# Performance work log

Hardware: AMD Instinct MI355X
Metric: run time of the kernel (lower is better)

## Reference

```python
import jax, jax.numpy as jnp
import numpy as np
from jax import lax

B, L, M, H = 8, 16, 256, 53
HID, NH, HD = 64, 4, 16  # hidden_size, n_heads, head_dim
ACT = 15  # 3 sub-actions x 5 categories


def _lstm_last(x, Wih, Whh, bih, bhh):
    # x: [N, T, D] batch_first; torch LSTM gate order i,f,g,o. Returns last hidden [N, HID].
    N = x.shape[0]
    h0 = jnp.zeros((N, HID), x.dtype)
    c0 = jnp.zeros((N, HID), x.dtype)
    def step(carry, xt):
        h, c = carry
        g = xt @ Wih.T + bih + h @ Whh.T + bhh
        i, f, gg, o = jnp.split(g, 4, axis=-1)
        c = jax.nn.sigmoid(f) * c + jax.nn.sigmoid(i) * jnp.tanh(gg)
        h = jax.nn.sigmoid(o) * jnp.tanh(c)
        return (h, c), None
    (h, _), _ = lax.scan(step, (h0, c0), x.transpose(1, 0, 2))
    return h


def setup_inputs():
    key = jax.random.key(0)
    ks = jax.random.split(key, 32)
    rn = lambda k, sh: (jax.random.normal(k, sh, jnp.float32) * 0.05)
    Gmat = jax.random.randint(ks[3], (M, M), 0, 2)
    Gmat = Gmat.at[jnp.arange(M), jnp.arange(M)].set(1)  # self-contact so no all-masked row
    return {
        'x_actor': jax.random.normal(ks[0], (B, L, M, H), jnp.float32),
        'x_critic': jax.random.normal(ks[1], (B, L, M, H), jnp.float32),
        'action': jax.random.randint(ks[2], (B, M, 3), 0, 5),
        'Gmat': Gmat,
        'Wa': rn(ks[4], (HID, H)), 'ba': jnp.zeros((HID,), jnp.float32),
        'Wg': rn(ks[5], (HID, H)), 'bg': jnp.zeros((HID,), jnp.float32),
        'Qw': rn(ks[6], (HID, HID)), 'Kw': rn(ks[7], (HID, HID)),
        'W2': rn(ks[8], (HID, 2 * HID)), 'b2': jnp.zeros((HID,), jnp.float32),
        'Wih_a': rn(ks[9], (4 * HID, HID)), 'Whh_a': rn(ks[10], (4 * HID, HID)),
        'bih_a': jnp.zeros((4 * HID,), jnp.float32), 'bhh_a': jnp.zeros((4 * HID,), jnp.float32),
        'Wih_c': rn(ks[11], (4 * HID, HID)), 'Whh_c': rn(ks[12], (4 * HID, HID)),
        'bih_c': jnp.zeros((4 * HID,), jnp.float32), 'bhh_c': jnp.zeros((4 * HID,), jnp.float32),
        'Wma1': rn(ks[13], (HID, HID)), 'bma1': jnp.zeros((HID,), jnp.float32),
        'Wma2': rn(ks[14], (ACT, HID)), 'bma2': jnp.zeros((ACT,), jnp.float32),
        'Wmc1': rn(ks[15], (HID, HID)), 'bmc1': jnp.zeros((HID,), jnp.float32),
        'Wmc2': rn(ks[16], (1, HID)), 'bmc2': jnp.zeros((1,), jnp.float32),
    }


def reference(x_actor, x_critic, action, Gmat, Wa, ba, Wg, bg, Qw, Kw, W2, b2,
              Wih_a, Whh_a, bih_a, bhh_a, Wih_c, Whh_c, bih_c, bhh_c,
              Wma1, bma1, Wma2, bma2, Wmc1, bmc1, Wmc2, bmc2):
    Bb, Ll, Mm, Hh = x_actor.shape
    xa = x_actor.transpose(1, 0, 2, 3).reshape(Ll * Bb, Mm, Hh)
    xc = xa  # original code overwrites x_critic with x_actor (preserved)
    a_lin = xa @ Wa.T + ba                               # [LB, M, HID]
    # --- GAT (GCN2) ---
    s = xc @ Wg.T + bg                                   # [LB, M, HID]
    q = (s @ Qw).reshape(-1, Mm, NH, HD)
    k = (s @ Kw).reshape(-1, Mm, NH, HD)
    s4 = s.reshape(-1, Mm, NH, HD)
    att = jnp.einsum('blhe,bshe->bhls', q, k) / jnp.asarray(128.0, s.dtype) ** 0.5
    att = jnp.where(Gmat > 0, att, jnp.asarray(-9e15, att.dtype))
    att = jax.nn.softmax(att, axis=-1)
    s_out = jnp.einsum('bshe,bhls->blhe', s4, att).reshape(-1, Mm, NH * HD)
    c_feat = jnp.concatenate([s, s_out], axis=-1) @ W2.T + b2  # [LB, M, HID]
    # --- to sequences [B*M, L, HID] ---
    xa_seq = a_lin.reshape(Ll, Bb * Mm, HID).transpose(1, 0, 2)
    xc_seq = c_feat.reshape(Ll, Bb * Mm, HID).transpose(1, 0, 2)
    ah = _lstm_last(xa_seq, Wih_a, Whh_a, bih_a, bhh_a)          # [B*M, HID]
    ch = _lstm_last(xc_seq, Wih_c, Whh_c, bih_c, bhh_c).reshape(Bb, Mm, HID)
    logits = (jnp.tanh(ah @ Wma1.T + bma1) @ Wma2.T + bma2).reshape(Bb, Mm, 3, 5)
    logp = jax.nn.log_softmax(logits, axis=-1)
    lp = jnp.take_along_axis(logp, action[..., None], axis=-1).squeeze(-1)  # [B,M,3]
    ent = -jnp.sum(jnp.exp(logp) * logp, axis=-1)                           # [B,M,3]
    value = jnp.tanh(ch @ Wmc1.T + bmc1) @ Wmc2.T + bmc2                    # [B,M,1]
    return (action, lp.sum(-1), ent.sum(-1), value)
```

## Files before the change

### kernel.cpp

```cpp
#include <hip/hip_runtime.h>
#include <math.h>

#define B_ 8
#define L_ 16
#define M_ 256
#define H_ 53
#define HID_ 64
#define LB_ 128
#define SCALE_ 0.08838834764831845f

typedef __attribute__((ext_vector_type(8))) short bf16x8;
typedef __attribute__((ext_vector_type(4))) float f32x4;

__device__ inline unsigned short f2bf(float f) {
  unsigned u = __builtin_bit_cast(unsigned, f);
  unsigned r = (u + 0x7FFFu + ((u >> 16) & 1u)) >> 16;
  return (unsigned short)r;
}
__device__ inline float sigm(float x) { return __builtin_amdgcn_rcpf(1.f + __expf(-x)); }
__device__ inline float ftanh(float x) { return 1.f - 2.f * __builtin_amdgcn_rcpf(1.f + __expf(2.f * x)); }

__global__ __launch_bounds__(256) void kP_pre(
    const float* __restrict__ Wg, const float* __restrict__ bg,
    const float* __restrict__ Qw, const float* __restrict__ Kw,
    const float* __restrict__ Wih_c, const float* __restrict__ W2,
    const float* __restrict__ b2, const int* __restrict__ Gmat,
    unsigned short* __restrict__ WQ_b, unsigned short* __restrict__ WK_b,
    float* __restrict__ bqk, unsigned short* __restrict__ Wfold_b,
    float* __restrict__ bias_fold, unsigned* __restrict__ gmask) {
  int blk = blockIdx.x, tid = threadIdx.x;
  if (blk < 128) {
    int idx = blk * 256 + tid;
    int n = idx >> 7, t = idx & 127;
    float acc = 0.f;
    for (int e = 0; e < 64; ++e) acc = fmaf(Wih_c[n * 64 + e], W2[e * 128 + t], acc);
    Wfold_b[idx] = f2bf(acc);
  } else if (blk < 160) {
    int idx = (blk - 128) * 256 + tid;
    int which = idx >> 12, n = (idx >> 6) & 63, j = idx & 63;
    const float* Mm = which ? Kw : Qw;
    float acc = 0.f;
    if (j < 53) {
      for (int e = 0; e < 64; ++e) acc = fmaf(Mm[e * 64 + n], Wg[e * 53 + j], acc);
      if (which == 0) acc *= SCALE_;
    }
    (which ? WK_b : WQ_b)[n * 64 + j] = f2bf(acc);
  } else if (blk == 160) {
    if (tid < 128) {
      int which = tid >> 6, n = tid & 63;
      const float* Mm = which ? Kw : Qw;
      float acc = 0.f;
      for (int e = 0; e < 64; ++e) acc = fmaf(bg[e], Mm[e * 64 + n], acc);
      if (which == 0) acc *= SCALE_;
      bqk[tid] = acc;
    }
  } else if (blk == 161) {
    float acc = 0.f;
    for (int e = 0; e < 64; ++e) acc = fmaf(Wih_c[tid * 64 + e], b2[e], acc);
    bias_fold[tid] = acc;
  } else {
    int w = tid >> 6, ln = tid & 63;
    int l = (blk - 162) * 4 + w;
    #pragma unroll
    for (int c = 0; c < 4; ++c) {
      int gv = Gmat[l * 256 + c * 64 + ln];
      unsigned long long msk = __ballot(gv > 0);
      if (ln == 0) {
        gmask[l * 8 + c * 2] = (unsigned)msk;
        gmask[l * 8 + c * 2 + 1] = (unsigned)(msk >> 32);
      }
    }
  }
}

#define XS 68
#define WS 68
#define OS 264
__global__ __launch_bounds__(256, 2) void kA_lin(const float* __restrict__ x,
    const float* __restrict__ Wa, const float* __restrict__ ba,
    const float* __restrict__ Wg, const float* __restrict__ bg,
    const unsigned short* __restrict__ WQ_b, const unsigned short* __restrict__ WK_b,
    const float* __restrict__ bqk,
    unsigned short* __restrict__ a_lin_bf, unsigned short* __restrict__ s_b,
    unsigned short* __restrict__ q_b, unsigned short* __restrict__ k_b,
    unsigned short* __restrict__ sT_b) {
  __shared__ __attribute__((aligned(16))) unsigned short x_lds[64 * XS];
  __shared__ __attribute__((aligned(16))) unsigned short w_lds[256 * WS];
  __shared__ float bias_lds[256];
  __shared__ __attribute__((aligned(16))) unsigned short out_lds[64 * OS];
  int tid = threadIdx.x;
  int row0 = blockIdx.x * 64;
  for (int i = tid; i < 64 * 64; i += 256) {
    int r = i >> 6, j = i & 63;
    int row = row0 + r;
    int lb = row >> 8, m = row & 255;
    int l = lb >> 3, b = lb & 7;
    float v = (j < 53) ? x[((b * L_ + l) * M_ + m) * H_ + j] : 0.f;
    x_lds[r * XS + j] = f2bf(v);
  }
  for (int i = tid; i < 64 * 64; i += 256) {
    int n = i >> 6, j = i & 63;
    w_lds[n * WS + j] = (j < 53) ? f2bf(Wa[n * 53 + j]) : 0;
    w_lds[(64 + n) * WS + j] = (j < 53) ? f2bf(Wg[n * 53 + j]) : 0;
    w_lds[(128 + n) * WS + j] = WQ_b[i];
    w_lds[(192 + n) * WS + j] = WK_b[i];
  }
  {
    float bv;
    if (tid < 64) bv = ba[tid];
    else if (tid < 128) bv = bg[tid - 64];
    else bv = bqk[tid - 128];
    bias_lds[tid] = bv;
  }
  __syncthreads();
  int lane = tid & 63, w = tid >> 6;
  int c16 = lane & 15, q4 = lane >> 4;
  bf16x8 a0 = *(const bf16x8*)&x_lds[(w * 16 + c16) * XS + q4 * 8];
  bf16x8 a1 = *(const bf16x8*)&x_lds[(w * 16 + c16) * XS + 32 + q4 * 8];
  #pragma unroll
  for (int nt = 0; nt < 16; ++nt) {
    bf16x8 b0 = *(const bf16x8*)&w_lds[(nt * 16 + c16) * WS + q4 * 8];
    bf16x8 b1 = *(const bf16x8*)&w_lds[(nt * 16 + c16) * WS + 32 + q4 * 8];
    float bs = bias_lds[nt * 16 + c16];
    f32x4 acc = {bs, bs, bs, bs};
    acc = __builtin_amdgcn_mfma_f32_16x16x32_bf16(a0, b0, acc, 0, 0, 0);
    acc = __builtin_amdgcn_mfma_f32_16x16x32_bf16(a1, b1, acc, 0, 0, 0);
    #pragma unroll
    for (int rr = 0; rr < 4; ++rr)
      out_lds[(w * 16 + q4 * 4 + rr) * OS + nt * 16 + c16] = f2bf(acc[rr]);
  }
  __syncthreads();
  for (int i = tid; i < 2048; i += 256) {
    int r = i >> 5, seg = i & 31;
    int which = seg >> 3, n8 = (seg & 7) * 8;
    uint4 v = *(const uint4*)&out_lds[r * OS + which * 64 + n8];
    unsigned short* dst = which == 0 ? a_lin_bf : which == 1 ? s_b : which == 2 ? q_b : k_b;
    *(uint4*)&dst[(row0 + r) * 64 + n8] = v;
  }
  int lb = row0 >> 8, m0 = row0 & 255;
  for (int i = tid; i < 1024; i += 256) {
    int e = i >> 4, mc = i & 15;
    ushort4 v;
    v.x = out_lds[(mc * 4 + 0) * OS + 64 + e];
    v.y = out_lds[(mc * 4 + 1) * OS + 64 + e];
    v.z = out_lds[(mc * 4 + 2) * OS + 64 + e];
    v.w = out_lds[(mc * 4 + 3) * OS + 64 + e];
    *(ushort4*)&sT_b[(lb * 64 + e) * 256 + m0 + mc * 4] = v;
  }
}

__global__ __launch_bounds__(512, 4) void kB_attn(
    const unsigned short* __restrict__ qb, const unsigned short* __restrict__ kb,
    const unsigned short* __restrict__ sT, const unsigned* __restrict__ gmask,
    unsigned short* __restrict__ so_b) {
  int blk = blockIdx.x;
  int lb = blk >> 2;
  int l0 = (blk & 3) << 6;
  int tid = threadIdx.x;
  int lane = tid & 63, w = tid >> 6;
  int c16 = lane & 15, q4 = lane >> 4;
  int lrow0 = (w >> 1) * 16;
  int h0 = (w & 1) * 2;
  int lrow = lb * 256 + l0 + lrow0;
  int kbase = lb * 256;
  const bf16x8 z8 = {0, 0, 0, 0, 0, 0, 0, 0};
  bf16x8 bq[2];
  #pragma unroll
  for (int hp = 0; hp < 2; ++hp) {
    int h = h0 + hp;
    bq[hp] = (q4 < 2) ? *(const bf16x8*)(qb + (lrow + c16) * 64 + h * 16 + q4 * 8) : z8;
  }
  unsigned gwv[8];
  #pragma unroll
  for (int sp = 0; sp < 8; ++sp) gwv[sp] = gmask[(l0 + lrow0 + c16) * 8 + sp];
  f32x4 accO[2];
  float sumh[2];
  #pragma unroll
  for (int hp = 0; hp < 2; ++hp) { accO[hp] = (f32x4){0.f, 0.f, 0.f, 0.f}; sumh[hp] = 0.f; }

  #pragma unroll
  for (int sp = 0; sp < 8; ++sp) {
    unsigned gw = gwv[sp];
    #pragma unroll
    for (int hp = 0; hp < 2; ++hp) {
      int h = h0 + hp;
      unsigned pk0A, pk1A, pk0B, pk1B;
      #pragma unroll
      for (int tp = 0; tp < 2; ++tp) {
        int t = sp * 2 + tp;
        bf16x8 ka = z8;
        if (q4 < 2) ka = *(const bf16x8*)(kb + (kbase + t * 16 + c16) * 64 + h * 16 + q4 * 8);
        f32x4 d = __builtin_amdgcn_mfma_f32_16x16x32_bf16(ka, bq[hp], (f32x4){0.f, 0.f, 0.f, 0.f}, 0, 0, 0);
        int bitbase = tp * 16 + q4 * 4;
        float p0 = ((gw >> (bitbase + 0)) & 1u) ? __expf(d[0]) : 0.f;
        float p1 = ((gw >> (bitbase + 1)) & 1u) ? __expf(d[1]) : 0.f;
        float p2 = ((gw >> (bitbase + 2)) & 1u) ? __expf(d[2]) : 0.f;
        float p3 = ((gw >> (bitbase + 3)) & 1u) ? __expf(d[3]) : 0.f;
        sumh[hp] += (p0 + p1) + (p2 + p3);
        unsigned lo = (unsigned)f2bf(p0) | ((unsigned)f2bf(p1) << 16);
        unsigned hi = (unsigned)f2bf(p2) | ((unsigned)f2bf(p3) << 16);
        if (tp == 0) { pk0A = lo; pk1A = hi; } else { pk0B = lo; pk1B = hi; }
      }
      int srcA = ((q4 & 1) * 2) * 16 + c16, srcB = srcA + 16;
      unsigned g0A = (unsigned)__shfl((int)pk0A, srcA);
      unsigned g1A = (unsigned)__shfl((int)pk1A, srcA);
      unsigned g2A = (unsigned)__shfl((int)pk0A, srcB);
      unsigned g3A = (unsigned)__shfl((int)pk1A, srcB);
      unsigned g0B = (unsigned)__shfl((int)pk0B, srcA);
      unsigned g1B = (unsigned)__shfl((int)pk1B, srcA);
      unsigned g2B = (unsigned)__shfl((int)pk0B, srcB);
      unsigned g3B = (unsigned)__shfl((int)pk1B, srcB);
      bool useB = (q4 >= 2);
      uint4 av;
      av.x = useB ? g0B : g0A;
      av.y = useB ? g1B : g1A;
      av.z = useB ? g2B : g2A;
      av.w = useB ? g3B : g3A;
      bf16x8 af = __builtin_bit_cast(bf16x8, av);
      bf16x8 bs = *(const bf16x8*)(sT + (lb * 64 + h * 16 + c16) * 256 + sp * 32 + q4 * 8);
      accO[hp] = __builtin_amdgcn_mfma_f32_16x16x32_bf16(af, bs, accO[hp], 0, 0, 0);
    }
  }
  #pragma unroll
  for (int hp = 0; hp < 2; ++hp) {
    int h = h0 + hp;
    float s = sumh[hp];
    s += __shfl_xor(s, 16);
    s += __shfl_xor(s, 32);
    #pragma unroll
    for (int r = 0; r < 4; ++r) {
      float sv = __shfl(s, q4 * 4 + r);
      float o = accO[hp][r] / sv;
      so_b[(lb * 256 + l0 + lrow0 + q4 * 4 + r) * 64 + h * 16 + c16] = f2bf(o);
    }
  }
}

__global__ __launch_bounds__(256, 1) void kR_lstm(
    const unsigned short* __restrict__ a_lin_bf,
    const unsigned short* __restrict__ s_b, const unsigned short* __restrict__ so_b,
    const unsigned short* __restrict__ Wfold_b, const float* __restrict__ bias_fold,
    const float* __restrict__ Wih_a,
    const float* __restrict__ Whh_a, const float* __restrict__ Whh_c,
    const float* __restrict__ bih_a, const float* __restrict__ bhh_a,
    const float* __restrict__ bih_c, const float* __restrict__ bhh_c,
    const int* __restrict__ action,
    const float* __restrict__ Wma1, const float* __restrict__ bma1,
    const float* __restrict__ Wma2, const float* __restrict__ bma2,
    const float* __restrict__ Wmc1, const float* __restrict__ bmc1,
    const float* __restrict__ Wmc2, const float* __restrict__ bmc2,
    float* __restrict__ out) {
  int blk = blockIdx.x;
  int which = blk >> 7, g = blk & 127;
  int seq0 = g * 16;
  int b = seq0 >> 8, m0 = seq0 & 255;
  __shared__ __attribute__((aligned(16))) unsigned short h_lds[2][16][72];
  __shared__ __attribute__((aligned(16))) unsigned short ha_lds[16][72];
  __shared__ float logit_lds[16][16];
  __shared__ float grp_lds[16][8];
  __shared__ float val_lds[16][4];
  int tid = threadIdx.x;
  int lane = tid & 63, w = tid >> 6;
  int c16 = lane & 15, q4 = lane >> 4;
  int hs0 = w * 16;
  const float* Whh = which ? Whh_c : Whh_a;
  const float* bih = which ? bih_c : bih_a;
  const float* bhh = which ? bhh_c : bhh_a;
  bf16x8 bwhh[4][2];
  float bias[4];
  #pragma unroll
  for (int nt = 0; nt < 4; ++nt) {
    int n = nt * 64 + hs0 + c16;
    bias[nt] = bih[n] + bhh[n] + (which ? bias_fold[n] : 0.f);
    #pragma unroll
    for (int kf = 0; kf < 2; ++kf) {
      const float* wp = Whh + n * 64 + kf * 32 + q4 * 8;
      bf16x8 bb;
      #pragma unroll
      for (int j = 0; j < 8; ++j) bb[j] = (short)f2bf(wp[j]);
      bwhh[nt][kf] = bb;
    }
  }
  for (int i = tid; i < 576; i += 256) ((unsigned*)h_lds)[i] = 0u;
  float cr[4] = {0.f, 0.f, 0.f, 0.f};
  const int STEP = 2048 * 64;
  __syncthreads();
  int cur = 0;
  if (which == 0) {
    bf16x8 bwin[4][2];
    #pragma unroll
    for (int nt = 0; nt < 4; ++nt) {
      int n = nt * 64 + hs0 + c16;
      #pragma unroll
      for (int kf = 0; kf < 2; ++kf) {
        const float* wp = Wih_a + n * 64 + kf * 32 + q4 * 8;
        bf16x8 bb;
        #pragma unroll
        for (int j = 0; j < 8; ++j) bb[j] = (short)f2bf(wp[j]);
        bwin[nt][kf] = bb;
      }
    }
    const unsigned short* inb = a_lin_bf + (b * 256 + m0 + c16) * 64;
    bf16x8 i0c = *(const bf16x8*)(inb + q4 * 8);
    bf16x8 i1c = *(const bf16x8*)(inb + 32 + q4 * 8);
    for (int l = 0; l < L_; ++l) {
      bf16x8 i0n = i0c, i1n = i1c;
      if (l < L_ - 1) {
        i0n = *(const bf16x8*)(inb + (l + 1) * STEP + q4 * 8);
        i1n = *(const bf16x8*)(inb + (l + 1) * STEP + 32 + q4 * 8);
      }
      bf16x8 ah0 = *(const bf16x8*)&h_lds[cur][c16][q4 * 8];
      bf16x8 ah1 = *(const bf16x8*)&h_lds[cur][c16][32 + q4 * 8];
      f32x4 acc[4];
      #pragma unroll
      for (int nt = 0; nt < 4; ++nt) {
        f32x4 a = {bias[nt], bias[nt], bias[nt], bias[nt]};
        a = __builtin_amdgcn_mfma_f32_16x16x32_bf16(i0c, bwin[nt][0], a, 0, 0, 0);
        a = __builtin_amdgcn_mfma_f32_16x16x32_bf16(i1c, bwin[nt][1], a, 0, 0, 0);
        a = __builtin_amdgcn_mfma_f32_16x16x32_bf16(ah0, bwhh[nt][0], a, 0, 0, 0);
        a = __builtin_amdgcn_mfma_f32_16x16x32_bf16(ah1, bwhh[nt][1], a, 0, 0, 0);
        acc[nt] = a;
      }
      #pragma unroll
      for (int rr = 0; rr < 4; ++rr) {
        float si = sigm(acc[0][rr]);
        float sf = sigm(acc[1][rr]);
        float gg = ftanh(acc[2][rr]);
        float so_ = sigm(acc[3][rr]);
        cr[rr] = sf * cr[rr] + si * gg;
        float hvv = so_ * ftanh(cr[rr]);
        h_lds[cur ^ 1][q4 * 4 + rr][hs0 + c16] = f2bf(hvv);
      }
      __syncthreads();
      cur ^= 1;
      i0c = i0n; i1c = i1n;
    }
  } else {
    bf16x8 bwf[4][4];
    #pragma unroll
    for (int nt = 0; nt < 4; ++nt) {
      int n = nt * 64 + hs0 + c16;
      #pragma unroll
      for (int kc = 0; kc < 4; ++kc) {
        bwf[nt][kc] = *(const bf16x8*)(Wfold_b + n * 128 + kc * 32 + q4 * 8);
      }
    }
    const unsigned short* sbB = s_b + (b * 256 + m0 + c16) * 64;
    const unsigned short* soB = so_b + (b * 256 + m0 + c16) * 64;
    bf16x8 s0c = *(const bf16x8*)(sbB + q4 * 8);
    bf16x8 s1c = *(const bf16x8*)(sbB + 32 + q4 * 8);
    bf16x8 o0c = *(const bf16x8*)(soB + q4 * 8);
    bf16x8 o1c = *(const bf16x8*)(soB + 32 + q4 * 8);
    for (int l = 0; l < L_; ++l) {
      bf16x8 s0n = s0c, s1n = s1c, o0n = o0c, o1n = o1c;
      if (l < L_ - 1) {
        s0n = *(const bf16x8*)(sbB + (l + 1) * STEP + q4 * 8);
        s1n = *(const bf16x8*)(sbB + (l + 1) * STEP + 32 + q4 * 8);
        o0n = *(const bf16x8*)(soB + (l + 1) * STEP + q4 * 8);
        o1n = *(const bf16x8*)(soB + (l + 1) * STEP + 32 + q4 * 8);
      }
      bf16x8 ah0 = *(const bf16x8*)&h_lds[cur][c16][q4 * 8];
      bf16x8 ah1 = *(const bf16x8*)&h_lds[cur][c16][32 + q4 * 8];
      f32x4 acc[4];
      #pragma unroll
      for (int nt = 0; nt < 4; ++nt) {
        f32x4 a = {bias[nt], bias[nt], bias[nt], bias[nt]};
        a = __builtin_amdgcn_mfma_f32_16x16x32_bf16(s0c, bwf[nt][0], a, 0, 0, 0);
        a = __builtin_amdgcn_mfma_f32_16x16x32_bf16(s1c, bwf[nt][1], a, 0, 0, 0);
        a = __builtin_amdgcn_mfma_f32_16x16x32_bf16(o0c, bwf[nt][2], a, 0, 0, 0);
        a = __builtin_amdgcn_mfma_f32_16x16x32_bf16(o1c, bwf[nt][3], a, 0, 0, 0);
        a = __builtin_amdgcn_mfma_f32_16x16x32_bf16(ah0, bwhh[nt][0], a, 0, 0, 0);
        a = __builtin_amdgcn_mfma_f32_16x16x32_bf16(ah1, bwhh[nt][1], a, 0, 0, 0);
        acc[nt] = a;
      }
      #pragma unroll
      for (int rr = 0; rr < 4; ++rr) {
        float si = sigm(acc[0][rr]);
        float sf = sigm(acc[1][rr]);
        float gg = ftanh(acc[2][rr]);
        float so_ = sigm(acc[3][rr]);
        cr[rr] = sf * cr[rr] + si * gg;
        float hvv = so_ * ftanh(cr[rr]);
        h_lds[cur ^ 1][q4 * 4 + rr][hs0 + c16] = f2bf(hvv);
      }
      __syncthreads();
      cur ^= 1;
      s0c = s0n; s1c = s1n; o0c = o0n; o1c = o1n;
    }
  }
  bf16x8 fh0 = *(const bf16x8*)&h_lds[cur][c16][q4 * 8];
  bf16x8 fh1 = *(const bf16x8*)&h_lds[cur][c16][32 + q4 * 8];
  if (which == 0) {
    bf16x8 bm1[2];
    #pragma unroll
    for (int kf = 0; kf < 2; ++kf) {
      const float* wp = Wma1 + (hs0 + c16) * 64 + kf * 32 + q4 * 8;
      bf16x8 bb;
      #pragma unroll
// ... 73 lines not shown
    acc = __builtin_amdgcn_mfma_f32_16x16x32_bf16(fh0, bm1[0], acc, 0, 0, 0);
    acc = __builtin_amdgcn_mfma_f32_16x16x32_bf16(fh1, bm1[1], acc, 0, 0, 0);
    float wv2 = Wmc2[hs0 + c16];
    float pv[4];
    #pragma unroll
    for (int rr = 0; rr < 4; ++rr) pv[rr] = ftanh(acc[rr]) * wv2;
    #pragma unroll
    for (int rr = 0; rr < 4; ++rr) {
      pv[rr] += __shfl_xor(pv[rr], 1);
      pv[rr] += __shfl_xor(pv[rr], 2);
      pv[rr] += __shfl_xor(pv[rr], 4);
      pv[rr] += __shfl_xor(pv[rr], 8);
    }
    if (c16 == 0) {
      #pragma unroll
      for (int rr = 0; rr < 4; ++rr) val_lds[q4 * 4 + rr][w] = pv[rr];
    }
    __syncthreads();
    if (tid < 16) {
      int n = seq0 + tid;
      out[10240 + n] = val_lds[tid][0] + val_lds[tid][1] + val_lds[tid][2] +
                       val_lds[tid][3] + bmc2[0];
    }
  }
}

extern "C" void kernel_launch(void* const* d_in, const int* in_sizes, int n_in,
                              void* d_out, int out_size, void* d_ws, size_t ws_size,
                              hipStream_t stream) {
  const float* x_actor = (const float*)d_in[0];
  const int* action = (const int*)d_in[2];
  const int* Gmat  = (const int*)d_in[3];
  const float* Wa = (const float*)d_in[4];  const float* ba = (const float*)d_in[5];
  const float* Wg = (const float*)d_in[6];  const float* bg = (const float*)d_in[7];
  const float* Qw = (const float*)d_in[8];  const float* Kw = (const float*)d_in[9];
  const float* W2 = (const float*)d_in[10]; const float* b2 = (const float*)d_in[11];
  const float* Wih_a = (const float*)d_in[12]; const float* Whh_a = (const float*)d_in[13];
  const float* bih_a = (const float*)d_in[14]; const float* bhh_a = (const float*)d_in[15];
  const float* Wih_c = (const float*)d_in[16]; const float* Whh_c = (const float*)d_in[17];
  const float* bih_c = (const float*)d_in[18]; const float* bhh_c = (const float*)d_in[19];
  const float* Wma1 = (const float*)d_in[20]; const float* bma1 = (const float*)d_in[21];
  const float* Wma2 = (const float*)d_in[22]; const float* bma2 = (const float*)d_in[23];
  const float* Wmc1 = (const float*)d_in[24]; const float* bmc1 = (const float*)d_in[25];
  const float* Wmc2 = (const float*)d_in[26]; const float* bmc2 = (const float*)d_in[27];

  unsigned short* us = (unsigned short*)d_ws;
  unsigned short* a_lin_bf = us;
  unsigned short* s_b  = us + 2097152;
  unsigned short* q_b  = us + 4194304;
  unsigned short* k_b  = us + 6291456;
  unsigned short* sT_b = us + 8388608;
  unsigned short* so_b = us + 10485760;
  unsigned short* Wfold_b = us + 12582912;
  unsigned short* WQ_b = us + 12615680;
  unsigned short* WK_b = us + 12619776;
  float* fb = (float*)(us + 12623872);
  float* bias_fold = fb;
  float* bqk = fb + 256;
  unsigned* gmask = (unsigned*)(fb + 384);
  float* out = (float*)d_out;

  kP_pre<<<226, 256, 0, stream>>>(Wg, bg, Qw, Kw, Wih_c, W2, b2, Gmat,
                                  WQ_b, WK_b, bqk, Wfold_b, bias_fold, gmask);
  kA_lin<<<512, 256, 0, stream>>>(x_actor, Wa, ba, Wg, bg, WQ_b, WK_b, bqk,
                                  a_lin_bf, s_b, q_b, k_b, sT_b);
  kB_attn<<<512, 512, 0, stream>>>(q_b, k_b, sT_b, gmask, so_b);
  kR_lstm<<<256, 256, 0, stream>>>(a_lin_bf, s_b, so_b, Wfold_b, bias_fold,
                                   Wih_a, Whh_a, Whh_c, bih_a, bhh_a, bih_c, bhh_c,
                                   action, Wma1, bma1, Wma2, bma2,
                                   Wmc1, bmc1, Wmc2, bmc2, out);
}
```

Before: 77.65 us.

## Fold preprocessing kernel into linear kernel, stage K/sT in LDS, pre-convert LSTM weights

Removes the separate kP_pre launch. Each kA_lin block now recomputes the Q/K-folded weights and biases itself with MFMA in LDS, and 205 extra blocks handle Wfold, gmask, bias_fold and the bf16 conversion of the LSTM weights. The attention kernel now stages the per-batch K and transposed S tiles in LDS instead of reading global memory repeatedly. The LSTM kernel loads pre-converted bf16 weights instead of converting fp32 in place. The cost is redundant per-block weight folding, larger LDS use that may cut occupancy in both kernels, and a new read-after-write dependency: gmask and the LSTM weights are produced by the same launch whose other blocks run concurrently, though they are only consumed by later launches.

```diff
diff --git a/kernel.cpp b/kernel.cpp
--- a/kernel.cpp
+++ b/kernel.cpp
@@ -17,135 +17,155 @@
   unsigned r = (u + 0x7FFFu + ((u >> 16) & 1u)) >> 16;
   return (unsigned short)r;
 }
+__device__ inline float bf2f(unsigned short u) {
+  unsigned v = ((unsigned)u) << 16;
+  return __builtin_bit_cast(float, v);
+}
 __device__ inline float sigm(float x) { return __builtin_amdgcn_rcpf(1.f + __expf(-x)); }
 __device__ inline float ftanh(float x) { return 1.f - 2.f * __builtin_amdgcn_rcpf(1.f + __expf(2.f * x)); }
 
-__global__ __launch_bounds__(256) void kP_pre(
-    const float* __restrict__ Wg, const float* __restrict__ bg,
-    const float* __restrict__ Qw, const float* __restrict__ Kw,
-    const float* __restrict__ Wih_c, const float* __restrict__ W2,
-    const float* __restrict__ b2, const int* __restrict__ Gmat,
-    unsigned short* __restrict__ WQ_b, unsigned short* __restrict__ WK_b,
-    float* __restrict__ bqk, unsigned short* __restrict__ Wfold_b,
-    float* __restrict__ bias_fold, unsigned* __restrict__ gmask) {
-  int blk = blockIdx.x, tid = threadIdx.x;
-  if (blk < 128) {
-    int idx = blk * 256 + tid;
-    int n = idx >> 7, t = idx & 127;
-    float acc = 0.f;
-    for (int e = 0; e < 64; ++e) acc = fmaf(Wih_c[n * 64 + e], W2[e * 128 + t], acc);
-    Wfold_b[idx] = f2bf(acc);
-  } else if (blk < 160) {
-    int idx = (blk - 128) * 256 + tid;
-    int which = idx >> 12, n = (idx >> 6) & 63, j = idx & 63;
-    const float* Mm = which ? Kw : Qw;
-    float acc = 0.f;
-    if (j < 53) {
-      for (int e = 0; e < 64; ++e) acc = fmaf(Mm[e * 64 + n], Wg[e * 53 + j], acc);
-      if (which == 0) acc *= SCALE_;
-    }
-    (which ? WK_b : WQ_b)[n * 64 + j] = f2bf(acc);
-  } else if (blk == 160) {
-    if (tid < 128) {
-      int which = tid >> 6, n = tid & 63;
-      const float* Mm = which ? Kw : Qw;
-      float acc = 0.f;
-      for (int e = 0; e < 64; ++e) acc = fmaf(bg[e], Mm[e * 64 + n], acc);
-      if (which == 0) acc *= SCALE_;
-      bqk[tid] = acc;
-    }
-  } else if (blk == 161) {
-    float acc = 0.f;
-    for (int e = 0; e < 64; ++e) acc = fmaf(Wih_c[tid * 64 + e], b2[e], acc);
-    bias_fold[tid] = acc;
-  } else {
-    int w = tid >> 6, ln = tid & 63;
-    int l = (blk - 162) * 4 + w;
-    #pragma unroll
-    for (int c = 0; c < 4; ++c) {
-      int gv = Gmat[l * 256 + c * 64 + ln];
-      unsigned long long msk = __ballot(gv > 0);
-      if (ln == 0) {
-        gmask[l * 8 + c * 2] = (unsigned)msk;
-        gmask[l * 8 + c * 2 + 1] = (unsigned)(msk >> 32);
-      }
-    }
-  }
-}
-
-#define XS 68
-#define WS 68
-#define OS 264
 __global__ __launch_bounds__(256, 2) void kA_lin(const float* __restrict__ x,
     const float* __restrict__ Wa, const float* __restrict__ ba,
     const float* __restrict__ Wg, const float* __restrict__ bg,
-    const unsigned short* __restrict__ WQ_b, const unsigned short* __restrict__ WK_b,
-    const float* __restrict__ bqk,
+    const float* __restrict__ Qw, const float* __restrict__ Kw,
+    const int* __restrict__ Gmat, const float* __restrict__ Wih_c,
+    const float* __restrict__ W2, const float* __restrict__ b2,
+    const float* __restrict__ Whh_a, const float* __restrict__ Whh_c,
+    const float* __restrict__ Wih_a,
     unsigned short* __restrict__ a_lin_bf, unsigned short* __restrict__ s_b,
     unsigned short* __restrict__ q_b, unsigned short* __restrict__ k_b,
-    unsigned short* __restrict__ sT_b) {
-  __shared__ __attribute__((aligned(16))) unsigned short x_lds[64 * XS];
-  __shared__ __attribute__((aligned(16))) unsigned short w_lds[256 * WS];
-  __shared__ float bias_lds[256];
-  __shared__ __attribute__((aligned(16))) unsigned short out_lds[64 * OS];
-  int tid = threadIdx.x;
-  int row0 = blockIdx.x * 64;
-  for (int i = tid; i < 64 * 64; i += 256) {
+    unsigned short* __restrict__ sT_b,
+    unsigned short* __restrict__ Wfold_b, float* __restrict__ bias_fold,
+    unsigned* __restrict__ gmask,
+    unsigned short* __restrict__ Whha_b, unsigned short* __restrict__ Whhc_b,
+    unsigned short* __restrict__ Wiha_b) {
+  int blk = blockIdx.x, tid = threadIdx.x;
+  if (blk >= 512) {
+    int b2k = blk - 512;
+    if (b2k < 128) {
+      int idx = b2k * 256 + tid;
+      int n = idx >> 7, t = idx & 127;
+      float acc = 0.f;
+      for (int e = 0; e < 64; ++e) acc = fmaf(Wih_c[n * 64 + e], W2[e * 128 + t], acc);
+      Wfold_b[idx] = f2bf(acc);
+    } else if (b2k < 192) {
+      int l = (b2k - 128) * 4 + (tid >> 6);
+      int ln = tid & 63;
+      #pragma unroll
+      for (int c = 0; c < 4; ++c) {
+        int gv = Gmat[l * 256 + c * 64 + ln];
+        unsigned long long msk = __ballot(gv > 0);
+        if (ln == 0) {
+          gmask[l * 8 + c * 2] = (unsigned)msk;
+          gmask[l * 8 + c * 2 + 1] = (unsigned)(msk >> 32);
+        }
+      }
+    } else if (b2k == 192) {
+      float acc = 0.f;
+      for (int e = 0; e < 64; ++e) acc = fmaf(Wih_c[tid * 64 + e], b2[e], acc);
+      bias_fold[tid] = acc;
+    } else {
+      int base = (b2k - 193) * 2048;
+      #pragma unroll
+      for (int k = 0; k < 8; ++k) {
+        int idx = base + k * 256 + tid;
+        if (idx < 16384) Whha_b[idx] = f2bf(Whh_a[idx]);
+        else if (idx < 32768) Whhc_b[idx - 16384] = f2bf(Whh_c[idx - 16384]);
+        else Wiha_b[idx - 32768] = f2bf(Wih_a[idx - 32768]);
+      }
+    }
+    return;
+  }
+  __shared__ __attribute__((aligned(16))) char smem[78848];
+  unsigned short* w_lds = (unsigned short*)smem;
+  unsigned short* x_lds = (unsigned short*)(smem + 34816);
+  float* bias_lds = (float*)(smem + 43520);
+  unsigned short* out_lds = (unsigned short*)(smem + 44544);
+  unsigned short* qwt = (unsigned short*)(smem + 44544);
+  unsigned short* kwt = (unsigned short*)(smem + 53248);
+  unsigned short* wgt = (unsigned short*)(smem + 61952);
+  int row0 = blk * 64;
+  for (int i = tid; i < 8192; i += 256) {
+    int n = i >> 6, j = i & 63;
+    float v = 0.f;
+    if (j < 53) v = (n < 64) ? Wa[n * 53 + j] : Wg[(n - 64) * 53 + j];
+    w_lds[n * 68 + j] = f2bf(v);
+  }
+  for (int i = tid; i < 4096; i += 256) {
     int r = i >> 6, j = i & 63;
     int row = row0 + r;
     int lb = row >> 8, m = row & 255;
     int l = lb >> 3, b = lb & 7;
     float v = (j < 53) ? x[((b * L_ + l) * M_ + m) * H_ + j] : 0.f;
-    x_lds[r * XS + j] = f2bf(v);
-  }
-  for (int i = tid; i < 64 * 64; i += 256) {
-    int n = i >> 6, j = i & 63;
-    w_lds[n * WS + j] = (j < 53) ? f2bf(Wa[n * 53 + j]) : 0;
-    w_lds[(64 + n) * WS + j] = (j < 53) ? f2bf(Wg[n * 53 + j]) : 0;
-    w_lds[(128 + n) * WS + j] = WQ_b[i];
-    w_lds[(192 + n) * WS + j] = WK_b[i];
-  }
-  {
-    float bv;
-    if (tid < 64) bv = ba[tid];
-    else if (tid < 128) bv = bg[tid - 64];
-    else bv = bqk[tid - 128];
-    bias_lds[tid] = bv;
-  }
+    x_lds[r * 68 + j] = f2bf(v);
+  }
+  for (int i = tid; i < 4096; i += 256) {
+    int a = i >> 6, e = i & 63;
+    qwt[a * 68 + e] = f2bf(Qw[e * 64 + a]);
+    kwt[a * 68 + e] = f2bf(Kw[e * 64 + a]);
+    wgt[a * 68 + e] = (a < 53) ? f2bf(Wg[e * 53 + a]) : (unsigned short)0;
+  }
+  if (tid < 128) bias_lds[tid] = (tid < 64) ? ba[tid] : bg[tid - 64];
   __syncthreads();
   int lane = tid & 63, w = tid >> 6;
   int c16 = lane & 15, q4 = lane >> 4;
-  bf16x8 a0 = *(const bf16x8*)&x_lds[(w * 16 + c16) * XS + q4 * 8];
-  bf16x8 a1 = *(const bf16x8*)&x_lds[(w * 16 + c16) * XS + 32 + q4 * 8];
+  #pragma unroll
+  for (int i = 0; i < 8; ++i) {
+    int tq = w * 8 + i;
+    int which = tq >> 4, rowt = (tq >> 2) & 3, colt = tq & 3;
+    const unsigned short* At = which ? kwt : qwt;
+    bf16x8 a0 = *(const bf16x8*)&At[(rowt * 16 + c16) * 68 + q4 * 8];
+    bf16x8 a1 = *(const bf16x8*)&At[(rowt * 16 + c16) * 68 + 32 + q4 * 8];
+    bf16x8 b0 = *(const bf16x8*)&wgt[(colt * 16 + c16) * 68 + q4 * 8];
+    bf16x8 b1 = *(const bf16x8*)&wgt[(colt * 16 + c16) * 68 + 32 + q4 * 8];
+    f32x4 acc = {0.f, 0.f, 0.f, 0.f};
+    acc = __builtin_amdgcn_mfma_f32_16x16x32_bf16(a0, b0, acc, 0, 0, 0);
+    acc = __builtin_amdgcn_mfma_f32_16x16x32_bf16(a1, b1, acc, 0, 0, 0);
+    float scl = which ? 1.f : SCALE_;
+    #pragma unroll
+    for (int rr = 0; rr < 4; ++rr)
+      w_lds[(128 + which * 64 + rowt * 16 + q4 * 4 + rr) * 68 + colt * 16 + c16] =
+          f2bf(acc[rr] * scl);
+  }
+  if (tid < 128) {
+    int which = tid >> 6, n = tid & 63;
+    const unsigned short* At = which ? kwt : qwt;
+    float acc = 0.f;
+    for (int e = 0; e < 64; ++e) acc = fmaf(bias_lds[64 + e], bf2f(At[n * 68 + e]), acc);
+    bias_lds[128 + tid] = which ? acc : acc * SCALE_;
+  }
+  __syncthreads();
+  bf16x8 xa0 = *(const bf16x8*)&x_lds[(w * 16 + c16) * 68 + q4 * 8];
+  bf16x8 xa1 = *(const bf16x8*)&x_lds[(w * 16 + c16) * 68 + 32 + q4 * 8];
   #pragma unroll
   for (int nt = 0; nt < 16; ++nt) {
-    bf16x8 b0 = *(const bf16x8*)&w_lds[(nt * 16 + c16) * WS + q4 * 8];
-    bf16x8 b1 = *(const bf16x8*)&w_lds[(nt * 16 + c16) * WS + 32 + q4 * 8];
+    bf16x8 b0 = *(const bf16x8*)&w_lds[(nt * 16 + c16) * 68 + q4 * 8];
+    bf16x8 b1 = *(const bf16x8*)&w_lds[(nt * 16 + c16) * 68 + 32 + q4 * 8];
     float bs = bias_lds[nt * 16 + c16];
     f32x4 acc = {bs, bs, bs, bs};
-    acc = __builtin_amdgcn_mfma_f32_16x16x32_bf16(a0, b0, acc, 0, 0, 0);
-    acc = __builtin_amdgcn_mfma_f32_16x16x32_bf16(a1, b1, acc, 0, 0, 0);
+    acc = __builtin_amdgcn_mfma_f32_16x16x32_bf16(xa0, b0, acc, 0, 0, 0);
+    acc = __builtin_amdgcn_mfma_f32_16x16x32_bf16(xa1, b1, acc, 0, 0, 0);
     #pragma unroll
     for (int rr = 0; rr < 4; ++rr)
-      out_lds[(w * 16 + q4 * 4 + rr) * OS + nt * 16 + c16] = f2bf(acc[rr]);
+      out_lds[(w * 16 + q4 * 4 + rr) * 268 + nt * 16 + c16] = f2bf(acc[rr]);
   }
   __syncthreads();
   for (int i = tid; i < 2048; i += 256) {
     int r = i >> 5, seg = i & 31;
     int which = seg >> 3, n8 = (seg & 7) * 8;
-    uint4 v = *(const uint4*)&out_lds[r * OS + which * 64 + n8];
+    uint4 v = *(const uint4*)&out_lds[r * 268 + which * 64 + n8];
     unsigned short* dst = which == 0 ? a_lin_bf : which == 1 ? s_b : which == 2 ? q_b : k_b;
     *(uint4*)&dst[(row0 + r) * 64 + n8] = v;
   }
-  int lb = row0 >> 8, m0 = row0 & 255;
+  int lbA = row0 >> 8, m0 = row0 & 255;
   for (int i = tid; i < 1024; i += 256) {
     int e = i >> 4, mc = i & 15;
     ushort4 v;
-    v.x = out_lds[(mc * 4 + 0) * OS + 64 + e];
-    v.y = out_lds[(mc * 4 + 1) * OS + 64 + e];
-    v.z = out_lds[(mc * 4 + 2) * OS + 64 + e];
-    v.w = out_lds[(mc * 4 + 3) * OS + 64 + e];
-    *(ushort4*)&sT_b[(lb * 64 + e) * 256 + m0 + mc * 4] = v;
+    v.x = out_lds[(mc * 4 + 0) * 268 + 64 + e];
+    v.y = out_lds[(mc * 4 + 1) * 268 + 64 + e];
+    v.z = out_lds[(mc * 4 + 2) * 268 + 64 + e];
+    v.w = out_lds[(mc * 4 + 3) * 268 + 64 + e];
+    *(ushort4*)&sT_b[(lbA * 64 + e) * 256 + m0 + mc * 4] = v;
   }
 }
 
@@ -153,16 +173,26 @@
     const unsigned short* __restrict__ qb, const unsigned short* __restrict__ kb,
     const unsigned short* __restrict__ sT, const unsigned* __restrict__ gmask,
     unsigned short* __restrict__ so_b) {
+  __shared__ __attribute__((aligned(16))) unsigned short k_lds[256 * 68];
+  __shared__ __attribute__((aligned(16))) unsigned short sT_lds[64 * 280];
   int blk = blockIdx.x;
   int lb = blk >> 2;
   int l0 = (blk & 3) << 6;
   int tid = threadIdx.x;
+  int kbase = lb * 256;
+  for (int i = tid; i < 2048; i += 512) {
+    int s = i >> 3, e8 = (i & 7) * 8;
+    *(uint4*)&k_lds[s * 68 + e8] = *(const uint4*)(kb + (kbase + s) * 64 + e8);
+  }
+  for (int i = tid; i < 2048; i += 512) {
+    int e = i >> 5, m8 = (i & 31) * 8;
+    *(uint4*)&sT_lds[e * 280 + m8] = *(const uint4*)(sT + (lb * 64 + e) * 256 + m8);
+  }
   int lane = tid & 63, w = tid >> 6;
   int c16 = lane & 15, q4 = lane >> 4;
   int lrow0 = (w >> 1) * 16;
   int h0 = (w & 1) * 2;
   int lrow = lb * 256 + l0 + lrow0;
-  int kbase = lb * 256;
   const bf16x8 z8 = {0, 0, 0, 0, 0, 0, 0, 0};
   bf16x8 bq[2];
   #pragma unroll
@@ -173,6 +203,7 @@
   unsigned gwv[8];
   #pragma unroll
   for (int sp = 0; sp < 8; ++sp) gwv[sp] = gmask[(l0 + lrow0 + c16) * 8 + sp];
+  __syncthreads();
   f32x4 accO[2];
   float sumh[2];
   #pragma unroll
@@ -189,7 +220,7 @@
       for (int tp = 0; tp < 2; ++tp) {
         int t = sp * 2 + tp;
         bf16x8 ka = z8;
-        if (q4 < 2) ka = *(const bf16x8*)(kb + (kbase + t * 16 + c16) * 64 + h * 16 + q4 * 8);
+        if (q4 < 2) ka = *(const bf16x8*)&k_lds[(t * 16 + c16) * 68 + h * 16 + q4 * 8];
         f32x4 d = __builtin_amdgcn_mfma_f32_16x16x32_bf16(ka, bq[hp], (f32x4){0.f, 0.f, 0.f, 0.f}, 0, 0, 0);
         int bitbase = tp * 16 + q4 * 4;
         float p0 = ((gw >> (bitbase + 0)) & 1u) ? __expf(d[0]) : 0.f;
@@ -217,7 +248,7 @@
       av.z = useB ? g2B : g2A;
       av.w = useB ? g3B : g3A;
       bf16x8 af = __builtin_bit_cast(bf16x8, av);
-      bf16x8 bs = *(const bf16x8*)(sT + (lb * 64 + h * 16 + c16) * 256 + sp * 32 + q4 * 8);
+      bf16x8 bs = *(const bf16x8*)&sT_lds[(h * 16 + c16) * 280 + sp * 32 + q4 * 8];
       accO[hp] = __builtin_amdgcn_mfma_f32_16x16x32_bf16(af, bs, accO[hp], 0, 0, 0);
     }
   }
@@ -240,8 +271,8 @@
     const unsigned short* __restrict__ a_lin_bf,
     const unsigned short* __restrict__ s_b, const unsigned short* __restrict__ so_b,
     const unsigned short* __restrict__ Wfold_b, const float* __restrict__ bias_fold,
-    const float* __restrict__ Wih_a,
-    const float* __restrict__ Whh_a, const float* __restrict__ Whh_c,
+    const unsigned short* __restrict__ Wiha_b,
+    const unsigned short* __restrict__ Whha_b, const unsigned short* __restrict__ Whhc_b,
     const float* __restrict__ bih_a, const float* __restrict__ bhh_a,
     const float* __restrict__ bih_c, const float* __restrict__ bhh_c,
     const int* __restrict__ action,
@@ -263,7 +294,7 @@
   int lane = tid & 63, w = tid >> 6;
   int c16 = lane & 15, q4 = lane >> 4;
   int hs0 = w * 16;
-  const float* Whh = which ? Whh_c : Whh_a;
+  const unsigned short* Whh_b = which ? Whhc_b : Whha_b;
   const float* bih = which ? bih_c : bih_a;
   const float* bhh = which ? bhh_c : bhh_a;
   bf16x8 bwhh[4][2];
@@ -273,13 +304,8 @@
     int n = nt * 64 + hs0 + c16;
     bias[nt] = bih[n] + bhh[n] + (which ? bias_fold[n] : 0.f);
     #pragma unroll
-    for (int kf = 0; kf < 2; ++kf) {
-      const float* wp = Whh + n * 64 + kf * 32 + q4 * 8;
-      bf16x8 bb;
-      #pragma unroll
-      for (int j = 0; j < 8; ++j) bb[j] = (short)f2bf(wp[j]);
-      bwhh[nt][kf] = bb;
-    }
+    for (int kf = 0; kf < 2; ++kf)
+      bwhh[nt][kf] = *(const bf16x8*)(Whh_b + n * 64 + kf * 32 + q4 * 8);
   }
   for (int i = tid; i < 576; i += 256) ((unsigned*)h_lds)[i] = 0u;
   float cr[4] = {0.f, 0.f, 0.f, 0.f};
@@ -292,13 +318,8 @@
     for (int nt = 0; nt < 4; ++nt) {
       int n = nt * 64 + hs0 + c16;
       #pragma unroll
-      for (int kf = 0; kf < 2; ++kf) {
-        const float* wp = Wih_a + n * 64 + kf * 32 + q4 * 8;
-        bf16x8 bb;
-        #pragma unroll
-        for (int j = 0; j < 8; ++j) bb[j] = (short)f2bf(wp[j]);
-        bwin[nt][kf] = bb;
-      }
+      for (int kf = 0; kf < 2; ++kf)
+        bwin[nt][kf] = *(const bf16x8*)(Wiha_b + n * 64 + kf * 32 + q4 * 8);
     }
     const unsigned short* inb = a_lin_bf + (b * 256 + m0 + c16) * 64;
     bf16x8 i0c = *(const bf16x8*)(inb + q4 * 8);
@@ -341,9 +362,8 @@
     for (int nt = 0; nt < 4; ++nt) {
       int n = nt * 64 + hs0 + c16;
       #pragma unroll
-      for (int kc = 0; kc < 4; ++kc) {
+      for (int kc = 0; kc < 4; ++kc)
         bwf[nt][kc] = *(const bf16x8*)(Wfold_b + n * 128 + kc * 32 + q4 * 8);
-      }
     }
     const unsigned short* sbB = s_b + (b * 256 + m0 + c16) * 64;
     const unsigned short* soB = so_b + (b * 256 + m0 + c16) * 64;
@@ -523,21 +543,23 @@
   unsigned short* sT_b = us + 8388608;
   unsigned short* so_b = us + 10485760;
   unsigned short* Wfold_b = us + 12582912;
-  unsigned short* WQ_b = us + 12615680;
-  unsigned short* WK_b = us + 12619776;
-  float* fb = (float*)(us + 12623872);
+  unsigned short* Whha_b  = us + 12615680;
+  unsigned short* Whhc_b  = us + 12632064;
+  unsigned short* Wiha_b  = us + 12648448;
+  float* fb = (float*)(us + 12664832);
   float* bias_fold = fb;
-  float* bqk = fb + 256;
-  unsigned* gmask = (unsigned*)(fb + 384);
+  unsigned* gmask = (unsigned*)(fb + 256);
   float* out = (float*)d_out;
 
-  kP_pre<<<226, 256, 0, stream>>>(Wg, bg, Qw, Kw, Wih_c, W2, b2, Gmat,
-                                  WQ_b, WK_b, bqk, Wfold_b, bias_fold, gmask);
-  kA_lin<<<512, 256, 0, stream>>>(x_actor, Wa, ba, Wg, bg, WQ_b, WK_b, bqk,
-                                  a_lin_bf, s_b, q_b, k_b, sT_b);
+  kA_lin<<<717, 256, 0, stream>>>(x_actor, Wa, ba, Wg, bg, Qw, Kw,
+                                  Gmat, Wih_c, W2, b2, Whh_a, Whh_c, Wih_a,
+                                  a_lin_bf, s_b, q_b, k_b, sT_b,
+                                  Wfold_b, bias_fold, gmask,
+                                  Whha_b, Whhc_b, Wiha_b);
   kB_attn<<<512, 512, 0, stream>>>(q_b, k_b, sT_b, gmask, so_b);
   kR_lstm<<<256, 256, 0, stream>>>(a_lin_bf, s_b, so_b, Wfold_b, bias_fold,
-                                   Wih_a, Whh_a, Whh_c, bih_a, bhh_a, bih_c, bhh_c,
+                                   Wiha_b, Whha_b, Whhc_b,
+                                   bih_a, bhh_a, bih_c, bhh_c,
                                    action, Wma1, bma1, Wma2, bma2,
                                    Wmc1, bmc1, Wmc2, bmc2, out);
 }
```

After: 90.97 us. 17.2% more time.

## Stage K and sT in LDS for attention, pre-convert LSTM weights, rebalance prep kernels

Applied to the files above, without the earlier changes.

The attention kernel now loads each batch's K (256x64) and transposed S tiles into padded shared memory once per block and reads MFMA operands from LDS instead of global memory. The Wfold, gmask and bias_fold precompute moves from kP_pre into extra blocks of kA_lin, which also pre-converts the LSTM Whh and Wih weights to bf16 so the recurrent kernel loads bf16x8 vectors directly instead of converting floats per thread. The out_lds padding also changes. The aim is less redundant global traffic and a shorter serial prep kernel, at the cost of more LDS per attention block (lower occupancy) and a larger kA_lin grid.

```diff
diff --git a/kernel.cpp b/kernel.cpp
--- a/kernel.cpp
+++ b/kernel.cpp
@@ -17,26 +17,21 @@
   unsigned r = (u + 0x7FFFu + ((u >> 16) & 1u)) >> 16;
   return (unsigned short)r;
 }
+__device__ inline float bf2f(unsigned short u) {
+  unsigned v = ((unsigned)u) << 16;
+  return __builtin_bit_cast(float, v);
+}
 __device__ inline float sigm(float x) { return __builtin_amdgcn_rcpf(1.f + __expf(-x)); }
 __device__ inline float ftanh(float x) { return 1.f - 2.f * __builtin_amdgcn_rcpf(1.f + __expf(2.f * x)); }
 
 __global__ __launch_bounds__(256) void kP_pre(
     const float* __restrict__ Wg, const float* __restrict__ bg,
     const float* __restrict__ Qw, const float* __restrict__ Kw,
-    const float* __restrict__ Wih_c, const float* __restrict__ W2,
-    const float* __restrict__ b2, const int* __restrict__ Gmat,
     unsigned short* __restrict__ WQ_b, unsigned short* __restrict__ WK_b,
-    float* __restrict__ bqk, unsigned short* __restrict__ Wfold_b,
-    float* __restrict__ bias_fold, unsigned* __restrict__ gmask) {
+    float* __restrict__ bqk) {
   int blk = blockIdx.x, tid = threadIdx.x;
-  if (blk < 128) {
+  if (blk < 32) {
     int idx = blk * 256 + tid;
-    int n = idx >> 7, t = idx & 127;
-    float acc = 0.f;
-    for (int e = 0; e < 64; ++e) acc = fmaf(Wih_c[n * 64 + e], W2[e * 128 + t], acc);
-    Wfold_b[idx] = f2bf(acc);
-  } else if (blk < 160) {
-    int idx = (blk - 128) * 256 + tid;
     int which = idx >> 12, n = (idx >> 6) & 63, j = idx & 63;
     const float* Mm = which ? Kw : Qw;
     float acc = 0.f;
@@ -45,7 +40,7 @@
       if (which == 0) acc *= SCALE_;
     }
     (which ? WK_b : WQ_b)[n * 64 + j] = f2bf(acc);
-  } else if (blk == 160) {
+  } else {
     if (tid < 128) {
       int which = tid >> 6, n = tid & 63;
       const float* Mm = which ? Kw : Qw;
@@ -54,42 +49,70 @@
       if (which == 0) acc *= SCALE_;
       bqk[tid] = acc;
     }
-  } else if (blk == 161) {
-    float acc = 0.f;
-    for (int e = 0; e < 64; ++e) acc = fmaf(Wih_c[tid * 64 + e], b2[e], acc);
-    bias_fold[tid] = acc;
-  } else {
-    int w = tid >> 6, ln = tid & 63;
-    int l = (blk - 162) * 4 + w;
-    #pragma unroll
-    for (int c = 0; c < 4; ++c) {
-      int gv = Gmat[l * 256 + c * 64 + ln];
-      unsigned long long msk = __ballot(gv > 0);
-      if (ln == 0) {
-        gmask[l * 8 + c * 2] = (unsigned)msk;
-        gmask[l * 8 + c * 2 + 1] = (unsigned)(msk >> 32);
-      }
-    }
   }
 }
 
 #define XS 68
 #define WS 68
-#define OS 264
+#define OS 268
 __global__ __launch_bounds__(256, 2) void kA_lin(const float* __restrict__ x,
     const float* __restrict__ Wa, const float* __restrict__ ba,
     const float* __restrict__ Wg, const float* __restrict__ bg,
     const unsigned short* __restrict__ WQ_b, const unsigned short* __restrict__ WK_b,
     const float* __restrict__ bqk,
+    const int* __restrict__ Gmat, const float* __restrict__ Wih_c,
+    const float* __restrict__ W2, const float* __restrict__ b2,
+    const float* __restrict__ Whh_a, const float* __restrict__ Whh_c,
+    const float* __restrict__ Wih_a,
     unsigned short* __restrict__ a_lin_bf, unsigned short* __restrict__ s_b,
     unsigned short* __restrict__ q_b, unsigned short* __restrict__ k_b,
-    unsigned short* __restrict__ sT_b) {
+    unsigned short* __restrict__ sT_b,
+    unsigned short* __restrict__ Wfold_b, float* __restrict__ bias_fold,
+    unsigned* __restrict__ gmask,
+    unsigned short* __restrict__ Whha_b, unsigned short* __restrict__ Whhc_b,
+    unsigned short* __restrict__ Wiha_b) {
+  int blk = blockIdx.x, tid = threadIdx.x;
+  if (blk >= 512) {
+    int b2k = blk - 512;
+    if (b2k < 128) {
+      int idx = b2k * 256 + tid;
+      int n = idx >> 7, t = idx & 127;
+      float acc = 0.f;
+      for (int e = 0; e < 64; ++e) acc = fmaf(Wih_c[n * 64 + e], W2[e * 128 + t], acc);
+      Wfold_b[idx] = f2bf(acc);
+    } else if (b2k < 192) {
+      int l = (b2k - 128) * 4 + (tid >> 6);
+      int ln = tid & 63;
+      #pragma unroll
+      for (int c = 0; c < 4; ++c) {
+        int gv = Gmat[l * 256 + c * 64 + ln];
+        unsigned long long msk = __ballot(gv > 0);
+        if (ln == 0) {
+          gmask[l * 8 + c * 2] = (unsigned)msk;
+          gmask[l * 8 + c * 2 + 1] = (unsigned)(msk >> 32);
+        }
+      }
+    } else if (b2k == 192) {
+      float acc = 0.f;
+      for (int e = 0; e < 64; ++e) acc = fmaf(Wih_c[tid * 64 + e], b2[e], acc);
+      bias_fold[tid] = acc;
+    } else {
+      int base = (b2k - 193) * 2048;
+      #pragma unroll
+      for (int k = 0; k < 8; ++k) {
+        int idx = base + k * 256 + tid;
+        if (idx < 16384) Whha_b[idx] = f2bf(Whh_a[idx]);
+        else if (idx < 32768) Whhc_b[idx - 16384] = f2bf(Whh_c[idx - 16384]);
+        else Wiha_b[idx - 32768] = f2bf(Wih_a[idx - 32768]);
+      }
+    }
+    return;
+  }
   __shared__ __attribute__((aligned(16))) unsigned short x_lds[64 * XS];
   __shared__ __attribute__((aligned(16))) unsigned short w_lds[256 * WS];
   __shared__ float bias_lds[256];
   __shared__ __attribute__((aligned(16))) unsigned short out_lds[64 * OS];
-  int tid = threadIdx.x;
-  int row0 = blockIdx.x * 64;
+  int row0 = blk * 64;
   for (int i = tid; i < 64 * 64; i += 256) {
     int r = i >> 6, j = i & 63;
     int row = row0 + r;
@@ -137,7 +160,7 @@
     unsigned short* dst = which == 0 ? a_lin_bf : which == 1 ? s_b : which == 2 ? q_b : k_b;
     *(uint4*)&dst[(row0 + r) * 64 + n8] = v;
   }
-  int lb = row0 >> 8, m0 = row0 & 255;
+  int lbA = row0 >> 8, m0 = row0 & 255;
   for (int i = tid; i < 1024; i += 256) {
     int e = i >> 4, mc = i & 15;
     ushort4 v;
@@ -145,7 +168,7 @@
     v.y = out_lds[(mc * 4 + 1) * OS + 64 + e];
     v.z = out_lds[(mc * 4 + 2) * OS + 64 + e];
     v.w = out_lds[(mc * 4 + 3) * OS + 64 + e];
-    *(ushort4*)&sT_b[(lb * 64 + e) * 256 + m0 + mc * 4] = v;
+    *(ushort4*)&sT_b[(lbA * 64 + e) * 256 + m0 + mc * 4] = v;
   }
 }
 
@@ -153,16 +176,26 @@
     const unsigned short* __restrict__ qb, const unsigned short* __restrict__ kb,
     const unsigned short* __restrict__ sT, const unsigned* __restrict__ gmask,
     unsigned short* __restrict__ so_b) {
+  __shared__ __attribute__((aligned(16))) unsigned short k_lds[256 * 68];
+  __shared__ __attribute__((aligned(16))) unsigned short sT_lds[64 * 280];
   int blk = blockIdx.x;
   int lb = blk >> 2;
   int l0 = (blk & 3) << 6;
   int tid = threadIdx.x;
+  int kbase = lb * 256;
+  for (int i = tid; i < 2048; i += 512) {
+    int s = i >> 3, e8 = (i & 7) * 8;
+    *(uint4*)&k_lds[s * 68 + e8] = *(const uint4*)(kb + (kbase + s) * 64 + e8);
+  }
+  for (int i = tid; i < 2048; i += 512) {
+    int e = i >> 5, m8 = (i & 31) * 8;
+    *(uint4*)&sT_lds[e * 280 + m8] = *(const uint4*)(sT + (lb * 64 + e) * 256 + m8);
+  }
   int lane = tid & 63, w = tid >> 6;
   int c16 = lane & 15, q4 = lane >> 4;
   int lrow0 = (w >> 1) * 16;
   int h0 = (w & 1) * 2;
   int lrow = lb * 256 + l0 + lrow0;
-  int kbase = lb * 256;
   const bf16x8 z8 = {0, 0, 0, 0, 0, 0, 0, 0};
   bf16x8 bq[2];
   #pragma unroll
@@ -173,6 +206,7 @@
   unsigned gwv[8];
   #pragma unroll
   for (int sp = 0; sp < 8; ++sp) gwv[sp] = gmask[(l0 + lrow0 + c16) * 8 + sp];
+  __syncthreads();
   f32x4 accO[2];
   float sumh[2];
   #pragma unroll
@@ -189,7 +223,7 @@
       for (int tp = 0; tp < 2; ++tp) {
         int t = sp * 2 + tp;
         bf16x8 ka = z8;
-        if (q4 < 2) ka = *(const bf16x8*)(kb + (kbase + t * 16 + c16) * 64 + h * 16 + q4 * 8);
+        if (q4 < 2) ka = *(const bf16x8*)&k_lds[(t * 16 + c16) * 68 + h * 16 + q4 * 8];
         f32x4 d = __builtin_amdgcn_mfma_f32_16x16x32_bf16(ka, bq[hp], (f32x4){0.f, 0.f, 0.f, 0.f}, 0, 0, 0);
         int bitbase = tp * 16 + q4 * 4;
         float p0 = ((gw >> (bitbase + 0)) & 1u) ? __expf(d[0]) : 0.f;
@@ -217,7 +251,7 @@
       av.z = useB ? g2B : g2A;
       av.w = useB ? g3B : g3A;
       bf16x8 af = __builtin_bit_cast(bf16x8, av);
-      bf16x8 bs = *(const bf16x8*)(sT + (lb * 64 + h * 16 + c16) * 256 + sp * 32 + q4 * 8);
+      bf16x8 bs = *(const bf16x8*)&sT_lds[(h * 16 + c16) * 280 + sp * 32 + q4 * 8];
       accO[hp] = __builtin_amdgcn_mfma_f32_16x16x32_bf16(af, bs, accO[hp], 0, 0, 0);
     }
   }
@@ -240,8 +274,8 @@
     const unsigned short* __restrict__ a_lin_bf,
     const unsigned short* __restrict__ s_b, const unsigned short* __restrict__ so_b,
     const unsigned short* __restrict__ Wfold_b, const float* __restrict__ bias_fold,
-    const float* __restrict__ Wih_a,
-    const float* __restrict__ Whh_a, const float* __restrict__ Whh_c,
+    const unsigned short* __restrict__ Wiha_b,
+    const unsigned short* __restrict__ Whha_b, const unsigned short* __restrict__ Whhc_b,
     const float* __restrict__ bih_a, const float* __restrict__ bhh_a,
     const float* __restrict__ bih_c, const float* __restrict__ bhh_c,
     const int* __restrict__ action,
@@ -263,7 +297,7 @@
   int lane = tid & 63, w = tid >> 6;
   int c16 = lane & 15, q4 = lane >> 4;
   int hs0 = w * 16;
-  const float* Whh = which ? Whh_c : Whh_a;
+  const unsigned short* Whh_b = which ? Whhc_b : Whha_b;
   const float* bih = which ? bih_c : bih_a;
   const float* bhh = which ? bhh_c : bhh_a;
   bf16x8 bwhh[4][2];
@@ -273,13 +307,8 @@
     int n = nt * 64 + hs0 + c16;
     bias[nt] = bih[n] + bhh[n] + (which ? bias_fold[n] : 0.f);
     #pragma unroll
-    for (int kf = 0; kf < 2; ++kf) {
-      const float* wp = Whh + n * 64 + kf * 32 + q4 * 8;
-      bf16x8 bb;
-      #pragma unroll
-      for (int j = 0; j < 8; ++j) bb[j] = (short)f2bf(wp[j]);
-      bwhh[nt][kf] = bb;
-    }
+    for (int kf = 0; kf < 2; ++kf)
+      bwhh[nt][kf] = *(const bf16x8*)(Whh_b + n * 64 + kf * 32 + q4 * 8);
   }
   for (int i = tid; i < 576; i += 256) ((unsigned*)h_lds)[i] = 0u;
   float cr[4] = {0.f, 0.f, 0.f, 0.f};
@@ -292,13 +321,8 @@
     for (int nt = 0; nt < 4; ++nt) {
       int n = nt * 64 + hs0 + c16;
       #pragma unroll
-      for (int kf = 0; kf < 2; ++kf) {
-        const float* wp = Wih_a + n * 64 + kf * 32 + q4 * 8;
-        bf16x8 bb;
-        #pragma unroll
-        for (int j = 0; j < 8; ++j) bb[j] = (short)f2bf(wp[j]);
-        bwin[nt][kf] = bb;
-      }
+      for (int kf = 0; kf < 2; ++kf)
+        bwin[nt][kf] = *(const bf16x8*)(Wiha_b + n * 64 + kf * 32 + q4 * 8);
     }
     const unsigned short* inb = a_lin_bf + (b * 256 + m0 + c16) * 64;
     bf16x8 i0c = *(const bf16x8*)(inb + q4 * 8);
@@ -341,9 +365,8 @@
     for (int nt = 0; nt < 4; ++nt) {
       int n = nt * 64 + hs0 + c16;
       #pragma unroll
-      for (int kc = 0; kc < 4; ++kc) {
+      for (int kc = 0; kc < 4; ++kc)
         bwf[nt][kc] = *(const bf16x8*)(Wfold_b + n * 128 + kc * 32 + q4 * 8);
-      }
     }
     const unsigned short* sbB = s_b + (b * 256 + m0 + c16) * 64;
     const unsigned short* soB = so_b + (b * 256 + m0 + c16) * 64;
@@ -523,21 +546,27 @@
   unsigned short* sT_b = us + 8388608;
   unsigned short* so_b = us + 10485760;
   unsigned short* Wfold_b = us + 12582912;
-  unsigned short* WQ_b = us + 12615680;
-  unsigned short* WK_b = us + 12619776;
-  float* fb = (float*)(us + 12623872);
+  unsigned short* Whha_b  = us + 12615680;
+  unsigned short* Whhc_b  = us + 12632064;
+  unsigned short* Wiha_b  = us + 12648448;
+  unsigned short* WQ_b    = us + 12664832;
+  unsigned short* WK_b    = us + 12668928;
+  float* fb = (float*)(us + 12673024);
   float* bias_fold = fb;
   float* bqk = fb + 256;
   unsigned* gmask = (unsigned*)(fb + 384);
   float* out = (float*)d_out;
 
-  kP_pre<<<226, 256, 0, stream>>>(Wg, bg, Qw, Kw, Wih_c, W2, b2, Gmat,
-                                  WQ_b, WK_b, bqk, Wfold_b, bias_fold, gmask);
-  kA_lin<<<512, 256, 0, stream>>>(x_actor, Wa, ba, Wg, bg, WQ_b, WK_b, bqk,
-                                  a_lin_bf, s_b, q_b, k_b, sT_b);
+  kP_pre<<<33, 256, 0, stream>>>(Wg, bg, Qw, Kw, WQ_b, WK_b, bqk);
+  kA_lin<<<729, 256, 0, stream>>>(x_actor, Wa, ba, Wg, bg, WQ_b, WK_b, bqk,
+                                  Gmat, Wih_c, W2, b2, Whh_a, Whh_c, Wih_a,
+                                  a_lin_bf, s_b, q_b, k_b, sT_b,
+                                  Wfold_b, bias_fold, gmask,
+                                  Whha_b, Whhc_b, Wiha_b);
   kB_attn<<<512, 512, 0, stream>>>(q_b, k_b, sT_b, gmask, so_b);
   kR_lstm<<<256, 256, 0, stream>>>(a_lin_bf, s_b, so_b, Wfold_b, bias_fold,
-                                   Wih_a, Whh_a, Whh_c, bih_a, bhh_a, bih_c, bhh_c,
+                                   Wiha_b, Whha_b, Whhc_b,
+                                   bih_a, bhh_a, bih_c, bhh_c,
                                    action, Wma1, bma1, Wma2, bma2,
                                    Wmc1, bmc1, Wmc2, bmc2, out);
 }
```

Measured after the change: 73.87 us. 1.05x faster.
